# Optimization experiments

Measured on AMD Instinct MI355X. Metric: run time of the kernel, lower is better.

The kernel has to match this reference:

```python
import jax, jax.numpy as jnp
from jax import lax
import numpy as np

B, I, T, H = 128, 512, 256, 1024


def setup_inputs() -> dict:
    key = jax.random.key(0)
    k1, k2, k3, k4, k5 = jax.random.split(key, 5)
    s = 1.0 / np.sqrt(H)  # PyTorch LSTM init scale
    return {
        "x": jax.random.normal(k1, (B, I, T), jnp.float32),
        "W_ih": jax.random.uniform(k2, (4 * H, I), jnp.float32, -s, s),
        "W_hh": jax.random.uniform(k3, (4 * H, H), jnp.float32, -s, s),
        "b_ih": jax.random.uniform(k4, (4 * H,), jnp.float32, -s, s),
        "b_hh": jax.random.uniform(k5, (4 * H,), jnp.float32, -s, s),
    }


def reference(x, W_ih, W_hh, b_ih, b_hh):
    # x: [B, I, T] -> module transposes to [B, T, I]; scan over time.
    xs = jnp.transpose(x, (2, 0, 1))  # [T, B, I]
    # Precompute input projections for all timesteps (one big GEMM).
    x_proj = jnp.einsum('tbi,gi->tbg', xs, W_ih) + b_ih + b_hh  # [T, B, 4H]
    H_ = W_hh.shape[1]

    def step(carry, xp):
        h, c = carry
        gates = xp + h @ W_hh.T  # [B, 4H]
        i, f, g, o = jnp.split(gates, 4, axis=-1)  # PyTorch gate order i,f,g,o
        i = jax.nn.sigmoid(i)
        f = jax.nn.sigmoid(f)
        g = jnp.tanh(g)
        o = jax.nn.sigmoid(o)
        c = f * c + i * g
        h = o * jnp.tanh(c)
        return (h, c), None

    h0 = jnp.zeros((x.shape[0], H_), x.dtype)
    (h, _), _ = lax.scan(step, (h0, h0), x_proj)
    return h  # [B, H] == h_t.squeeze(0)
```

## Files before the change

kernel.cpp:

```cpp
#include <hip/hip_runtime.h>
#include <hip/hip_bf16.h>
#include <cstdint>
#include <cstddef>

#define B_ 128
#define I_ 512
#define T_ 256
#define H_ 1024

typedef __attribute__((ext_vector_type(8))) short short8;
typedef __attribute__((ext_vector_type(4))) float floatx4;

static __device__ __forceinline__ unsigned short f2bf(float f) {
  unsigned u = __float_as_uint(f);
  u += 0x7FFFu + ((u >> 16) & 1u);
  return (unsigned short)(u >> 16);
}
static __device__ __forceinline__ short8 pack_bf8(floatx4 a, floatx4 b) {
  short8 v;
  v[0] = (short)f2bf(a[0]); v[1] = (short)f2bf(a[1]);
  v[2] = (short)f2bf(a[2]); v[3] = (short)f2bf(a[3]);
  v[4] = (short)f2bf(b[0]); v[5] = (short)f2bf(b[1]);
  v[6] = (short)f2bf(b[2]); v[7] = (short)f2bf(b[3]);
  return v;
}

__global__ void __launch_bounds__(256) k_transpose(
    const float* __restrict__ x, unsigned short* __restrict__ xs) {
  __shared__ float tile[64][65];
  const int b  = blockIdx.x;
  const int i0 = blockIdx.y * 64;
  const int t0 = blockIdx.z * 64;
  const int tid = threadIdx.x;
  const int c = tid & 63, r4 = tid >> 6;
  const float* src = x + (size_t)b * I_ * T_ + (size_t)i0 * T_ + t0;
#pragma unroll
  for (int it = 0; it < 16; ++it) {
    const int r = it * 4 + r4;
    tile[r][c] = src[(size_t)r * T_ + c];
  }
  __syncthreads();
#pragma unroll
  for (int it = 0; it < 16; ++it) {
    const int tr = it * 4 + r4;
    xs[((size_t)(t0 + tr) * B_ + b) * I_ + i0 + c] = f2bf(tile[c][tr]);
  }
}

__global__ void __launch_bounds__(256, 1) k_lstm(
    const unsigned short* __restrict__ xs,
    const float* __restrict__ Whh,
    const float* __restrict__ Wih,
    const float* __restrict__ bih,
    const float* __restrict__ bhh,
    unsigned short* __restrict__ hring,
    float* __restrict__ out,
    unsigned int* __restrict__ flags)
{
  extern __shared__ char smem[];
  unsigned short (*hst)[32][264] = (unsigned short (*)[32][264])smem;
  float (*gx)[32][17] = (float (*)[32][17])(smem + 101376);

  const int wg = blockIdx.x, tid = threadIdx.x;
  const int lane = tid & 63, wave = tid >> 6;
  const int bt = wg & 3, jt = wg >> 2;
  const int b0 = bt * 32, j0 = jt * 16;
  const int quad = lane >> 4, cr = lane & 15;
  const size_t HBUF = (size_t)B_ * H_;

  short8 whf[32];
  {
    const float* wrow = Whh + (size_t)(wave * H_ + j0 + cr) * H_;
#pragma unroll
    for (int ks = 0; ks < 32; ++ks) {
      floatx4 wa = *(const floatx4*)(wrow + ks * 32 + quad * 8);
      floatx4 wb = *(const floatx4*)(wrow + ks * 32 + quad * 8 + 4);
      whf[ks] = pack_bf8(wa, wb);
    }
  }
  short8 wif[16];
  {
    const float* irow = Wih + (size_t)(wave * H_ + j0 + cr) * I_;
#pragma unroll
    for (int ks = 0; ks < 16; ++ks) {
      floatx4 wa = *(const floatx4*)(irow + ks * 32 + quad * 8);
      floatx4 wb = *(const floatx4*)(irow + ks * 32 + quad * 8 + 4);
      wif[ks] = pack_bf8(wa, wb);
    }
  }

  const int eb = tid >> 3;
  const int ejp = tid & 7;
  float bias[4][2];
#pragma unroll
  for (int q = 0; q < 4; ++q)
#pragma unroll
    for (int jj = 0; jj < 2; ++jj)
      bias[q][jj] = bih[q * H_ + j0 + ejp * 2 + jj] + bhh[q * H_ + j0 + ejp * 2 + jj];

  const int srow = tid >> 3;
  const int sq = tid & 7;

  float c0 = 0.f, c1 = 0.f;

  for (int t = 0; t < T_; ++t) {
    const unsigned short* hin = hring + (size_t)t * HBUF;
    unsigned short* hout = hring + (size_t)((t + 1) & 255) * HBUF;
    const unsigned short* xrow = xs + ((size_t)t * B_ + b0 + srow) * I_ + sq * 8;
    const unsigned short* hrow = hin + (size_t)(b0 + srow) * H_ + sq * 8;

    short8 xv[8];
#pragma unroll
    for (int c2 = 0; c2 < 2; ++c2)
#pragma unroll
      for (int p = 0; p < 4; ++p)
        xv[c2 * 4 + p] = *(const short8*)(xrow + c2 * 256 + p * 64);
#pragma unroll
    for (int c2 = 0; c2 < 2; ++c2)
#pragma unroll
      for (int p = 0; p < 4; ++p)
        *(short8*)&hst[c2][srow][sq * 8 + p * 64] = xv[c2 * 4 + p];
    __syncthreads();

    floatx4 accx0 = {0.f,0.f,0.f,0.f}, accx1 = {0.f,0.f,0.f,0.f};
    floatx4 aha0 = {0.f,0.f,0.f,0.f}, aha1 = {0.f,0.f,0.f,0.f};
    floatx4 ahb0 = {0.f,0.f,0.f,0.f}, ahb1 = {0.f,0.f,0.f,0.f};

    if (t > 0 && wave == 0) {
      const unsigned tgt = (unsigned)t;
      for (;;) {
        unsigned v = __hip_atomic_load(&flags[(bt + 4 * lane) * 16],
                                       __ATOMIC_RELAXED, __HIP_MEMORY_SCOPE_AGENT);
        if (__ballot(v >= tgt) == ~0ull) break;
        __builtin_amdgcn_s_sleep(1);
      }
    }

#pragma unroll
    for (int c2 = 0; c2 < 2; ++c2)
#pragma unroll
      for (int ks8 = 0; ks8 < 8; ++ks8) {
        short8 a0 = *(const short8*)&hst[c2][cr][ks8 * 32 + quad * 8];
        short8 a1 = *(const short8*)&hst[c2][16 + cr][ks8 * 32 + quad * 8];
        accx0 = __builtin_amdgcn_mfma_f32_16x16x32_bf16(a0, wif[c2 * 8 + ks8], accx0, 0, 0, 0);
        accx1 = __builtin_amdgcn_mfma_f32_16x16x32_bf16(a1, wif[c2 * 8 + ks8], accx1, 0, 0, 0);
      }
    __syncthreads();

    if (t > 0) {
      short8 hv8[16];
#pragma unroll
      for (int k = 0; k < 16; ++k)
        hv8[k] = *(const short8*)(hrow + (k >> 2) * 256 + (k & 3) * 64);

#pragma unroll
      for (int ch = 0; ch < 4; ++ch)
#pragma unroll
        for (int p = 0; p < 4; ++p)
          *(short8*)&hst[2 + ch][srow][sq * 8 + p * 64] = hv8[ch * 4 + p];
      __syncthreads();
#pragma unroll
      for (int ch = 0; ch < 4; ++ch)
#pragma unroll
        for (int ks8 = 0; ks8 < 8; ++ks8) {
          short8 a0 = *(const short8*)&hst[2 + ch][cr][ks8 * 32 + quad * 8];
          short8 a1 = *(const short8*)&hst[2 + ch][16 + cr][ks8 * 32 + quad * 8];
          if (ch < 2) {
            aha0 = __builtin_amdgcn_mfma_f32_16x16x32_bf16(a0, whf[ch * 8 + ks8], aha0, 0, 0, 0);
            aha1 = __builtin_amdgcn_mfma_f32_16x16x32_bf16(a1, whf[ch * 8 + ks8], aha1, 0, 0, 0);
          } else {
            ahb0 = __builtin_amdgcn_mfma_f32_16x16x32_bf16(a0, whf[ch * 8 + ks8], ahb0, 0, 0, 0);
            ahb1 = __builtin_amdgcn_mfma_f32_16x16x32_bf16(a1, whf[ch * 8 + ks8], ahb1, 0, 0, 0);
          }
        }
    }

#pragma unroll
    for (int r = 0; r < 4; ++r) {
      gx[wave][quad * 4 + r][cr]      = accx0[r] + aha0[r] + ahb0[r];
      gx[wave][16 + quad * 4 + r][cr] = accx1[r] + aha1[r] + ahb1[r];
    }
    __syncthreads();

    float hv0 = 0.f, hv1 = 0.f;
#pragma unroll
    for (int jj = 0; jj < 2; ++jj) {
      const int j = ejp * 2 + jj;
      float gi = gx[0][eb][j] + bias[0][jj];
      float gf = gx[1][eb][j] + bias[1][jj];
      float gg = gx[2][eb][j] + bias[2][jj];
      float go = gx[3][eb][j] + bias[3][jj];
      float si = 1.f / (1.f + __expf(-gi));
      float sf = 1.f / (1.f + __expf(-gf));
      float tg = 2.f / (1.f + __expf(-2.f * gg)) - 1.f;
      float so = 1.f / (1.f + __expf(-go));
      float& cc = jj ? c1 : c0;
      cc = sf * cc + si * tg;
      float th = 2.f / (1.f + __expf(-2.f * cc)) - 1.f;
      float hv = so * th;
      if (jj == 0) hv0 = hv; else hv1 = hv;
    }
    const unsigned hpack = (unsigned)f2bf(hv0) | ((unsigned)f2bf(hv1) << 16);
    __hip_atomic_store((unsigned*)(hout + (size_t)(b0 + eb) * H_ + j0 + ejp * 2),
                       hpack, __ATOMIC_RELAXED, __HIP_MEMORY_SCOPE_AGENT);
    if (t == T_ - 1) {
      out[(size_t)(b0 + eb) * H_ + j0 + ejp * 2 + 0] = hv0;
      out[(size_t)(b0 + eb) * H_ + j0 + ejp * 2 + 1] = hv1;
    }

    __syncthreads();
    if (tid == 0)
      __hip_atomic_store(&flags[wg * 16], (unsigned)(t + 1), __ATOMIC_RELAXED,
                         __HIP_MEMORY_SCOPE_AGENT);
  }
}

extern "C" void kernel_launch(void* const* d_in, const int* in_sizes, int n_in,
                              void* d_out, int out_size, void* d_ws, size_t ws_size,
                              hipStream_t stream) {
  (void)in_sizes; (void)n_in; (void)out_size; (void)ws_size;
  const float* x   = (const float*)d_in[0];
  const float* Wih = (const float*)d_in[1];
  const float* Whh = (const float*)d_in[2];
  const float* bih = (const float*)d_in[3];
  const float* bhh = (const float*)d_in[4];
  float* out = (float*)d_out;

  char* ws = (char*)d_ws;
  unsigned short* xs = (unsigned short*)ws;
  unsigned int*   fl = (unsigned int*)  (ws + 33554432);
  unsigned short* hring = (unsigned short*)d_in[0];

  hipMemsetAsync(fl, 0, 16384, stream);

  k_transpose<<<dim3(B_, I_ / 64, T_ / 64), 256, 0, stream>>>(x, xs);

  const int LDS_TOTAL = 110080;
  hipFuncSetAttribute((const void*)k_lstm,
                      hipFuncAttributeMaxDynamicSharedMemorySize, LDS_TOTAL);
  k_lstm<<<dim3(256), dim3(256), LDS_TOTAL, stream>>>(
      xs, Whh, Wih, bih, bhh, hring, out, fl);
}
```

Baseline: 1.158 ms.

## Split K across waves, load MFMA fragments directly from global, prefetch x

Each wave now owns a quarter of the K dimension for all four gates, instead of one gate over the full K. A-fragments for x and h are read straight from global memory into registers rather than staged through LDS, and partial sums are reduced through a small shared array in the gate stage. The next timestep's x fragment is prefetched before the flag wait, every wave polls the flags, and the flags are packed contiguously per batch tile. This removes several LDS round-trips and barriers per step on the serial recurrence path, at the cost of a larger cross-wave reduction and uncoalesced global fragment loads.

After: 1.402 ms. +21.0%, slower.

```diff
diff --git a/kernel.cpp b/kernel.cpp
--- a/kernel.cpp
+++ b/kernel.cpp
@@ -57,9 +57,7 @@
     float* __restrict__ out,
     unsigned int* __restrict__ flags)
 {
-  extern __shared__ char smem[];
-  unsigned short (*hst)[32][264] = (unsigned short (*)[32][264])smem;
-  float (*gx)[32][17] = (float (*)[32][17])(smem + 101376);
+  __shared__ float gx[4][32][67];
 
   const int wg = blockIdx.x, tid = threadIdx.x;
   const int lane = tid & 63, wave = tid >> 6;
@@ -67,25 +65,25 @@
   const int b0 = bt * 32, j0 = jt * 16;
   const int quad = lane >> 4, cr = lane & 15;
   const size_t HBUF = (size_t)B_ * H_;
-
-  short8 whf[32];
-  {
-    const float* wrow = Whh + (size_t)(wave * H_ + j0 + cr) * H_;
-#pragma unroll
-    for (int ks = 0; ks < 32; ++ks) {
+  const size_t XSTEP = (size_t)B_ * I_;
+
+  short8 whf[4][8];
+  short8 wif[4][4];
+#pragma unroll
+  for (int q = 0; q < 4; ++q) {
+    const float* wrow = Whh + (size_t)(q * H_ + j0 + cr) * H_ + wave * 256;
+#pragma unroll
+    for (int ks = 0; ks < 8; ++ks) {
       floatx4 wa = *(const floatx4*)(wrow + ks * 32 + quad * 8);
       floatx4 wb = *(const floatx4*)(wrow + ks * 32 + quad * 8 + 4);
-      whf[ks] = pack_bf8(wa, wb);
-    }
-  }
-  short8 wif[16];
-  {
-    const float* irow = Wih + (size_t)(wave * H_ + j0 + cr) * I_;
-#pragma unroll
-    for (int ks = 0; ks < 16; ++ks) {
+      whf[q][ks] = pack_bf8(wa, wb);
+    }
+    const float* irow = Wih + (size_t)(q * H_ + j0 + cr) * I_ + wave * 128;
+#pragma unroll
+    for (int ks = 0; ks < 4; ++ks) {
       floatx4 wa = *(const floatx4*)(irow + ks * 32 + quad * 8);
       floatx4 wb = *(const floatx4*)(irow + ks * 32 + quad * 8 + 4);
-      wif[ks] = pack_bf8(wa, wb);
+      wif[q][ks] = pack_bf8(wa, wb);
     }
   }
 
@@ -98,108 +96,100 @@
     for (int jj = 0; jj < 2; ++jj)
       bias[q][jj] = bih[q * H_ + j0 + ejp * 2 + jj] + bhh[q * H_ + j0 + ejp * 2 + jj];
 
-  const int srow = tid >> 3;
-  const int sq = tid & 7;
+  const unsigned short* xfrag =
+      xs + (size_t)(b0 + cr) * I_ + wave * 128 + quad * 8;
+
+  short8 xv[2][4];
+#pragma unroll
+  for (int hh = 0; hh < 2; ++hh)
+#pragma unroll
+    for (int ks = 0; ks < 4; ++ks)
+      xv[hh][ks] = *(const short8*)(xfrag + (size_t)hh * 16 * I_ + ks * 32);
 
   float c0 = 0.f, c1 = 0.f;
 
   for (int t = 0; t < T_; ++t) {
-    const unsigned short* hin = hring + (size_t)t * HBUF;
-    unsigned short* hout = hring + (size_t)((t + 1) & 255) * HBUF;
-    const unsigned short* xrow = xs + ((size_t)t * B_ + b0 + srow) * I_ + sq * 8;
-    const unsigned short* hrow = hin + (size_t)(b0 + srow) * H_ + sq * 8;
-
-    short8 xv[8];
-#pragma unroll
-    for (int c2 = 0; c2 < 2; ++c2)
-#pragma unroll
-      for (int p = 0; p < 4; ++p)
-        xv[c2 * 4 + p] = *(const short8*)(xrow + c2 * 256 + p * 64);
-#pragma unroll
-    for (int c2 = 0; c2 < 2; ++c2)
-#pragma unroll
-      for (int p = 0; p < 4; ++p)
-        *(short8*)&hst[c2][srow][sq * 8 + p * 64] = xv[c2 * 4 + p];
-    __syncthreads();
-
-    floatx4 accx0 = {0.f,0.f,0.f,0.f}, accx1 = {0.f,0.f,0.f,0.f};
-    floatx4 aha0 = {0.f,0.f,0.f,0.f}, aha1 = {0.f,0.f,0.f,0.f};
-    floatx4 ahb0 = {0.f,0.f,0.f,0.f}, ahb1 = {0.f,0.f,0.f,0.f};
-
-    if (t > 0 && wave == 0) {
+    floatx4 acc[4][2];
+#pragma unroll
+    for (int q = 0; q < 4; ++q) {
+      acc[q][0] = (floatx4){0.f, 0.f, 0.f, 0.f};
+      acc[q][1] = (floatx4){0.f, 0.f, 0.f, 0.f};
+    }
+
+#pragma unroll
+    for (int ks = 0; ks < 4; ++ks)
+#pragma unroll
+      for (int q = 0; q < 4; ++q) {
+        acc[q][0] = __builtin_amdgcn_mfma_f32_16x16x32_bf16(xv[0][ks], wif[q][ks], acc[q][0], 0, 0, 0);
+        acc[q][1] = __builtin_amdgcn_mfma_f32_16x16x32_bf16(xv[1][ks], wif[q][ks], acc[q][1], 0, 0, 0);
+      }
+
+    if (t + 1 < T_) {
+      const unsigned short* xp = xfrag + (size_t)(t + 1) * XSTEP;
+#pragma unroll
+      for (int hh = 0; hh < 2; ++hh)
+#pragma unroll
+        for (int ks = 0; ks < 4; ++ks)
+          xv[hh][ks] = *(const short8*)(xp + (size_t)hh * 16 * I_ + ks * 32);
+    }
+
+    if (t > 0) {
       const unsigned tgt = (unsigned)t;
       for (;;) {
-        unsigned v = __hip_atomic_load(&flags[(bt + 4 * lane) * 16],
+        unsigned v = __hip_atomic_load(&flags[bt * 64 + lane],
                                        __ATOMIC_RELAXED, __HIP_MEMORY_SCOPE_AGENT);
         if (__ballot(v >= tgt) == ~0ull) break;
         __builtin_amdgcn_s_sleep(1);
       }
-    }
-
-#pragma unroll
-    for (int c2 = 0; c2 < 2; ++c2)
-#pragma unroll
-      for (int ks8 = 0; ks8 < 8; ++ks8) {
-        short8 a0 = *(const short8*)&hst[c2][cr][ks8 * 32 + quad * 8];
-        short8 a1 = *(const short8*)&hst[c2][16 + cr][ks8 * 32 + quad * 8];
-        accx0 = __builtin_amdgcn_mfma_f32_16x16x32_bf16(a0, wif[c2 * 8 + ks8], accx0, 0, 0, 0);
-        accx1 = __builtin_amdgcn_mfma_f32_16x16x32_bf16(a1, wif[c2 * 8 + ks8], accx1, 0, 0, 0);
+      asm volatile("" ::: "memory");
+
+      const unsigned short* hf = hring + (size_t)t * HBUF +
+          (size_t)(b0 + cr) * H_ + wave * 256 + quad * 8;
+      short8 hv[2][8];
+#pragma unroll
+      for (int hh = 0; hh < 2; ++hh)
+#pragma unroll
+        for (int ks = 0; ks < 8; ++ks)
+          hv[hh][ks] = *(const short8*)(hf + (size_t)hh * 16 * H_ + ks * 32);
+
+#pragma unroll
+      for (int ks = 0; ks < 8; ++ks)
+#pragma unroll
+        for (int q = 0; q < 4; ++q) {
+          acc[q][0] = __builtin_amdgcn_mfma_f32_16x16x32_bf16(hv[0][ks], whf[q][ks], acc[q][0], 0, 0, 0);
+          acc[q][1] = __builtin_amdgcn_mfma_f32_16x16x32_bf16(hv[1][ks], whf[q][ks], acc[q][1], 0, 0, 0);
+        }
+    }
+
+#pragma unroll
+    for (int q = 0; q < 4; ++q)
+#pragma unroll
+      for (int r = 0; r < 4; ++r) {
+        gx[wave][quad * 4 + r][q * 16 + cr]      = acc[q][0][r];
+        gx[wave][16 + quad * 4 + r][q * 16 + cr] = acc[q][1][r];
       }
     __syncthreads();
 
-    if (t > 0) {
-      short8 hv8[16];
-#pragma unroll
-      for (int k = 0; k < 16; ++k)
-        hv8[k] = *(const short8*)(hrow + (k >> 2) * 256 + (k & 3) * 64);
-
-#pragma unroll
-      for (int ch = 0; ch < 4; ++ch)
-#pragma unroll
-        for (int p = 0; p < 4; ++p)
-          *(short8*)&hst[2 + ch][srow][sq * 8 + p * 64] = hv8[ch * 4 + p];
-      __syncthreads();
-#pragma unroll
-      for (int ch = 0; ch < 4; ++ch)
-#pragma unroll
-        for (int ks8 = 0; ks8 < 8; ++ks8) {
-          short8 a0 = *(const short8*)&hst[2 + ch][cr][ks8 * 32 + quad * 8];
-          short8 a1 = *(const short8*)&hst[2 + ch][16 + cr][ks8 * 32 + quad * 8];
-          if (ch < 2) {
-            aha0 = __builtin_amdgcn_mfma_f32_16x16x32_bf16(a0, whf[ch * 8 + ks8], aha0, 0, 0, 0);
-            aha1 = __builtin_amdgcn_mfma_f32_16x16x32_bf16(a1, whf[ch * 8 + ks8], aha1, 0, 0, 0);
-          } else {
-            ahb0 = __builtin_amdgcn_mfma_f32_16x16x32_bf16(a0, whf[ch * 8 + ks8], ahb0, 0, 0, 0);
-            ahb1 = __builtin_amdgcn_mfma_f32_16x16x32_bf16(a1, whf[ch * 8 + ks8], ahb1, 0, 0, 0);
-          }
-        }
-    }
-
-#pragma unroll
-    for (int r = 0; r < 4; ++r) {
-      gx[wave][quad * 4 + r][cr]      = accx0[r] + aha0[r] + ahb0[r];
-      gx[wave][16 + quad * 4 + r][cr] = accx1[r] + aha1[r] + ahb1[r];
-    }
-    __syncthreads();
-
     float hv0 = 0.f, hv1 = 0.f;
 #pragma unroll
     for (int jj = 0; jj < 2; ++jj) {
       const int j = ejp * 2 + jj;
-      float gi = gx[0][eb][j] + bias[0][jj];
-      float gf = gx[1][eb][j] + bias[1][jj];
-      float gg = gx[2][eb][j] + bias[2][jj];
-      float go = gx[3][eb][j] + bias[3][jj];
-      float si = 1.f / (1.f + __expf(-gi));
-      float sf = 1.f / (1.f + __expf(-gf));
-      float tg = 2.f / (1.f + __expf(-2.f * gg)) - 1.f;
-      float so = 1.f / (1.f + __expf(-go));
+      float g[4];
+#pragma unroll
+      for (int q = 0; q < 4; ++q)
+        g[q] = gx[0][eb][q * 16 + j] + gx[1][eb][q * 16 + j] +
+               gx[2][eb][q * 16 + j] + gx[3][eb][q * 16 + j] + bias[q][jj];
+      float si = 1.f / (1.f + __expf(-g[0]));
+      float sf = 1.f / (1.f + __expf(-g[1]));
+      float tg = 2.f / (1.f + __expf(-2.f * g[2])) - 1.f;
+      float so = 1.f / (1.f + __expf(-g[3]));
       float& cc = jj ? c1 : c0;
       cc = sf * cc + si * tg;
       float th = 2.f / (1.f + __expf(-2.f * cc)) - 1.f;
-      float hv = so * th;
-      if (jj == 0) hv0 = hv; else hv1 = hv;
-    }
+      float hvv = so * th;
+      if (jj == 0) hv0 = hvv; else hv1 = hvv;
+    }
+    unsigned short* hout = hring + (size_t)((t + 1) & 255) * HBUF;
     const unsigned hpack = (unsigned)f2bf(hv0) | ((unsigned)f2bf(hv1) << 16);
     __hip_atomic_store((unsigned*)(hout + (size_t)(b0 + eb) * H_ + j0 + ejp * 2),
                        hpack, __ATOMIC_RELAXED, __HIP_MEMORY_SCOPE_AGENT);
@@ -210,8 +200,8 @@
 
     __syncthreads();
     if (tid == 0)
-      __hip_atomic_store(&flags[wg * 16], (unsigned)(t + 1), __ATOMIC_RELAXED,
-                         __HIP_MEMORY_SCOPE_AGENT);
+      __hip_atomic_store(&flags[bt * 64 + jt], (unsigned)(t + 1),
+                         __ATOMIC_RELAXED, __HIP_MEMORY_SCOPE_AGENT);
   }
 }
 
@@ -235,9 +225,6 @@
 
   k_transpose<<<dim3(B_, I_ / 64, T_ / 64), 256, 0, stream>>>(x, xs);
 
-  const int LDS_TOTAL = 110080;
-  hipFuncSetAttribute((const void*)k_lstm,
-                      hipFuncAttributeMaxDynamicSharedMemorySize, LDS_TOTAL);
-  k_lstm<<<dim3(256), dim3(256), LDS_TOTAL, stream>>>(
+  k_lstm<<<dim3(256), dim3(256), 0, stream>>>(
       xs, Whh, Wih, bih, bhh, hring, out, fl);
 }
```

## Use per-wave completion flags, prefetch next-step x, and drop barriers in LSTM loop

Applied to the files above, without the earlier changes.

Each wave now publishes its own completion flag after waiting for its stores to drain, rather than the whole workgroup barriering before thread 0 publishes. Every wave spins on its own producers' flags, and the recurrent h loads are issued right after that wait so they overlap with the input-projection MFMAs. Next-timestep x rows are prefetched into registers one step ahead, and two __syncthreads per step are removed. This shortens the per-timestep serial critical path. In exchange it causes four times more flag polling traffic and relies on relaxed atomics plus manual waitcnt for cross-workgroup ordering.

Result: slower. 1.516 ms (+30.9%).

```diff
diff --git a/kernel.cpp b/kernel.cpp
--- a/kernel.cpp
+++ b/kernel.cpp
@@ -67,6 +67,7 @@
   const int b0 = bt * 32, j0 = jt * 16;
   const int quad = lane >> 4, cr = lane & 15;
   const size_t HBUF = (size_t)B_ * H_;
+  const size_t XSTEP = (size_t)B_ * I_;
 
   short8 whf[32];
   {
@@ -101,39 +102,57 @@
   const int srow = tid >> 3;
   const int sq = tid & 7;
 
+  const unsigned short* xbase = xs + (size_t)(b0 + srow) * I_ + sq * 8;
+
+  short8 xv[8];
+#pragma unroll
+  for (int c2 = 0; c2 < 2; ++c2)
+#pragma unroll
+    for (int p = 0; p < 4; ++p)
+      xv[c2 * 4 + p] = *(const short8*)(xbase + c2 * 256 + p * 64);
+
   float c0 = 0.f, c1 = 0.f;
 
   for (int t = 0; t < T_; ++t) {
-    const unsigned short* hin = hring + (size_t)t * HBUF;
-    unsigned short* hout = hring + (size_t)((t + 1) & 255) * HBUF;
-    const unsigned short* xrow = xs + ((size_t)t * B_ + b0 + srow) * I_ + sq * 8;
-    const unsigned short* hrow = hin + (size_t)(b0 + srow) * H_ + sq * 8;
-
-    short8 xv[8];
-#pragma unroll
-    for (int c2 = 0; c2 < 2; ++c2)
-#pragma unroll
-      for (int p = 0; p < 4; ++p)
-        xv[c2 * 4 + p] = *(const short8*)(xrow + c2 * 256 + p * 64);
 #pragma unroll
     for (int c2 = 0; c2 < 2; ++c2)
 #pragma unroll
       for (int p = 0; p < 4; ++p)
         *(short8*)&hst[c2][srow][sq * 8 + p * 64] = xv[c2 * 4 + p];
+    if (t + 1 < T_) {
+      const unsigned short* xp = xbase + (size_t)(t + 1) * XSTEP;
+#pragma unroll
+      for (int c2 = 0; c2 < 2; ++c2)
+#pragma unroll
+        for (int p = 0; p < 4; ++p)
+          xv[c2 * 4 + p] = *(const short8*)(xp + c2 * 256 + p * 64);
+    }
     __syncthreads();
 
     floatx4 accx0 = {0.f,0.f,0.f,0.f}, accx1 = {0.f,0.f,0.f,0.f};
     floatx4 aha0 = {0.f,0.f,0.f,0.f}, aha1 = {0.f,0.f,0.f,0.f};
     floatx4 ahb0 = {0.f,0.f,0.f,0.f}, ahb1 = {0.f,0.f,0.f,0.f};
 
-    if (t > 0 && wave == 0) {
+    short8 hv8[16];
+    if (t > 0) {
       const unsigned tgt = (unsigned)t;
+      const unsigned int* fb = flags + (size_t)(bt + 4 * lane) * 16;
       for (;;) {
-        unsigned v = __hip_atomic_load(&flags[(bt + 4 * lane) * 16],
-                                       __ATOMIC_RELAXED, __HIP_MEMORY_SCOPE_AGENT);
-        if (__ballot(v >= tgt) == ~0ull) break;
+        unsigned v0 = __hip_atomic_load(fb + 0, __ATOMIC_RELAXED, __HIP_MEMORY_SCOPE_AGENT);
+        unsigned v1 = __hip_atomic_load(fb + 1, __ATOMIC_RELAXED, __HIP_MEMORY_SCOPE_AGENT);
+        unsigned v2 = __hip_atomic_load(fb + 2, __ATOMIC_RELAXED, __HIP_MEMORY_SCOPE_AGENT);
+        unsigned v3 = __hip_atomic_load(fb + 3, __ATOMIC_RELAXED, __HIP_MEMORY_SCOPE_AGENT);
+        bool ok = (v0 >= tgt) & (v1 >= tgt) & (v2 >= tgt) & (v3 >= tgt);
+        if (__ballot(ok) == ~0ull) break;
         __builtin_amdgcn_s_sleep(1);
       }
+      asm volatile("" ::: "memory");
+
+      const unsigned short* hrow = hring + (size_t)t * HBUF +
+                                   (size_t)(b0 + srow) * H_ + sq * 8;
+#pragma unroll
+      for (int k = 0; k < 16; ++k)
+        hv8[k] = *(const short8*)(hrow + (k >> 2) * 256 + (k & 3) * 64);
     }
 
 #pragma unroll
@@ -145,14 +164,8 @@
         accx0 = __builtin_amdgcn_mfma_f32_16x16x32_bf16(a0, wif[c2 * 8 + ks8], accx0, 0, 0, 0);
         accx1 = __builtin_amdgcn_mfma_f32_16x16x32_bf16(a1, wif[c2 * 8 + ks8], accx1, 0, 0, 0);
       }
-    __syncthreads();
 
     if (t > 0) {
-      short8 hv8[16];
-#pragma unroll
-      for (int k = 0; k < 16; ++k)
-        hv8[k] = *(const short8*)(hrow + (k >> 2) * 256 + (k & 3) * 64);
-
 #pragma unroll
       for (int ch = 0; ch < 4; ++ch)
 #pragma unroll
@@ -200,6 +213,7 @@
       float hv = so * th;
       if (jj == 0) hv0 = hv; else hv1 = hv;
     }
+    unsigned short* hout = hring + (size_t)((t + 1) & 255) * HBUF;
     const unsigned hpack = (unsigned)f2bf(hv0) | ((unsigned)f2bf(hv1) << 16);
     __hip_atomic_store((unsigned*)(hout + (size_t)(b0 + eb) * H_ + j0 + ejp * 2),
                        hpack, __ATOMIC_RELAXED, __HIP_MEMORY_SCOPE_AGENT);
@@ -208,10 +222,10 @@
       out[(size_t)(b0 + eb) * H_ + j0 + ejp * 2 + 1] = hv1;
     }
 
-    __syncthreads();
-    if (tid == 0)
-      __hip_atomic_store(&flags[wg * 16], (unsigned)(t + 1), __ATOMIC_RELAXED,
-                         __HIP_MEMORY_SCOPE_AGENT);
+    asm volatile("s_waitcnt vmcnt(0)" ::: "memory");
+    if (lane == 0)
+      __hip_atomic_store(&flags[wg * 16 + wave], (unsigned)(t + 1),
+                         __ATOMIC_RELAXED, __HIP_MEMORY_SCOPE_AGENT);
   }
 }
 
```

## Switch LSTM recurrence to 32x32x16 MFMA with split-K across wave pairs

Applied to the files above, without the earlier changes.

Replaces the 16x16x32 bf16 MFMA tiles with 32x32x16 MFMAs. Each wave now computes two gates over 32 batch rows for half of the K dimension, and the partial sums from the wave pairs are reduced through LDS in the gate nonlinearity stage. The aim is to halve the LDS A-operand reads per wave and use the larger MFMA shape for better throughput on the serial per-step critical path. The gx buffer grows to hold 32 columns, which raises LDS use, and each gate now needs an extra cross-wave add.

Result: faster. 1.079 ms (-6.9%).

```diff
diff --git a/kernel.cpp b/kernel.cpp
--- a/kernel.cpp
+++ b/kernel.cpp
@@ -10,6 +10,7 @@
 
 typedef __attribute__((ext_vector_type(8))) short short8;
 typedef __attribute__((ext_vector_type(4))) float floatx4;
+typedef __attribute__((ext_vector_type(16))) float floatx16;
 
 static __device__ __forceinline__ unsigned short f2bf(float f) {
   unsigned u = __float_as_uint(f);
@@ -23,6 +24,10 @@
   v[4] = (short)f2bf(b[0]); v[5] = (short)f2bf(b[1]);
   v[6] = (short)f2bf(b[2]); v[7] = (short)f2bf(b[3]);
   return v;
+}
+static __device__ __forceinline__ floatx16 zero16() {
+  return (floatx16){0.f,0.f,0.f,0.f,0.f,0.f,0.f,0.f,
+                    0.f,0.f,0.f,0.f,0.f,0.f,0.f,0.f};
 }
 
 __global__ void __launch_bounds__(256) k_transpose(
@@ -59,33 +64,37 @@
 {
   extern __shared__ char smem[];
   unsigned short (*hst)[32][264] = (unsigned short (*)[32][264])smem;
-  float (*gx)[32][17] = (float (*)[32][17])(smem + 101376);
+  float (*gx)[32][33] = (float (*)[32][33])(smem + 101376);
 
   const int wg = blockIdx.x, tid = threadIdx.x;
   const int lane = tid & 63, wave = tid >> 6;
+  const int gp = wave >> 1, kh = wave & 1;
   const int bt = wg & 3, jt = wg >> 2;
   const int b0 = bt * 32, j0 = jt * 16;
-  const int quad = lane >> 4, cr = lane & 15;
+  const int arow = lane & 31;
+  const int hi = lane >> 5;
+  const int gate = gp * 2 + (arow >> 4);
+  const int wcol = j0 + (arow & 15);
   const size_t HBUF = (size_t)B_ * H_;
 
   short8 whf[32];
   {
-    const float* wrow = Whh + (size_t)(wave * H_ + j0 + cr) * H_;
-#pragma unroll
-    for (int ks = 0; ks < 32; ++ks) {
-      floatx4 wa = *(const floatx4*)(wrow + ks * 32 + quad * 8);
-      floatx4 wb = *(const floatx4*)(wrow + ks * 32 + quad * 8 + 4);
-      whf[ks] = pack_bf8(wa, wb);
+    const float* wrow = Whh + (size_t)(gate * H_ + wcol) * H_ + kh * 512;
+#pragma unroll
+    for (int kc = 0; kc < 32; ++kc) {
+      floatx4 wa = *(const floatx4*)(wrow + kc * 16 + hi * 8);
+      floatx4 wb = *(const floatx4*)(wrow + kc * 16 + hi * 8 + 4);
+      whf[kc] = pack_bf8(wa, wb);
     }
   }
   short8 wif[16];
   {
-    const float* irow = Wih + (size_t)(wave * H_ + j0 + cr) * I_;
-#pragma unroll
-    for (int ks = 0; ks < 16; ++ks) {
-      floatx4 wa = *(const floatx4*)(irow + ks * 32 + quad * 8);
-      floatx4 wb = *(const floatx4*)(irow + ks * 32 + quad * 8 + 4);
-      wif[ks] = pack_bf8(wa, wb);
+    const float* irow = Wih + (size_t)(gate * H_ + wcol) * I_ + kh * 256;
+#pragma unroll
+    for (int kc = 0; kc < 16; ++kc) {
+      floatx4 wa = *(const floatx4*)(irow + kc * 16 + hi * 8);
+      floatx4 wb = *(const floatx4*)(irow + kc * 16 + hi * 8 + 4);
+      wif[kc] = pack_bf8(wa, wb);
     }
   }
 
@@ -122,9 +131,8 @@
         *(short8*)&hst[c2][srow][sq * 8 + p * 64] = xv[c2 * 4 + p];
     __syncthreads();
 
-    floatx4 accx0 = {0.f,0.f,0.f,0.f}, accx1 = {0.f,0.f,0.f,0.f};
-    floatx4 aha0 = {0.f,0.f,0.f,0.f}, aha1 = {0.f,0.f,0.f,0.f};
-    floatx4 ahb0 = {0.f,0.f,0.f,0.f}, ahb1 = {0.f,0.f,0.f,0.f};
+    floatx16 accxa = zero16(), accxb = zero16();
+    floatx16 ah0 = zero16(), ah1 = zero16();
 
     if (t > 0 && wave == 0) {
       const unsigned tgt = (unsigned)t;
@@ -137,14 +145,13 @@
     }
 
 #pragma unroll
-    for (int c2 = 0; c2 < 2; ++c2)
-#pragma unroll
-      for (int ks8 = 0; ks8 < 8; ++ks8) {
-        short8 a0 = *(const short8*)&hst[c2][cr][ks8 * 32 + quad * 8];
-        short8 a1 = *(const short8*)&hst[c2][16 + cr][ks8 * 32 + quad * 8];
-        accx0 = __builtin_amdgcn_mfma_f32_16x16x32_bf16(a0, wif[c2 * 8 + ks8], accx0, 0, 0, 0);
-        accx1 = __builtin_amdgcn_mfma_f32_16x16x32_bf16(a1, wif[c2 * 8 + ks8], accx1, 0, 0, 0);
-      }
+    for (int kc = 0; kc < 16; ++kc) {
+      short8 a = *(const short8*)&hst[kh][arow][kc * 16 + hi * 8];
+      if (kc & 1)
+        accxb = __builtin_amdgcn_mfma_f32_32x32x16_bf16(a, wif[kc], accxb, 0, 0, 0);
+      else
+        accxa = __builtin_amdgcn_mfma_f32_32x32x16_bf16(a, wif[kc], accxa, 0, 0, 0);
+    }
     __syncthreads();
 
     if (t > 0) {
@@ -160,25 +167,21 @@
           *(short8*)&hst[2 + ch][srow][sq * 8 + p * 64] = hv8[ch * 4 + p];
       __syncthreads();
 #pragma unroll
-      for (int ch = 0; ch < 4; ++ch)
-#pragma unroll
-        for (int ks8 = 0; ks8 < 8; ++ks8) {
-          short8 a0 = *(const short8*)&hst[2 + ch][cr][ks8 * 32 + quad * 8];
-          short8 a1 = *(const short8*)&hst[2 + ch][16 + cr][ks8 * 32 + quad * 8];
-          if (ch < 2) {
-            aha0 = __builtin_amdgcn_mfma_f32_16x16x32_bf16(a0, whf[ch * 8 + ks8], aha0, 0, 0, 0);
-            aha1 = __builtin_amdgcn_mfma_f32_16x16x32_bf16(a1, whf[ch * 8 + ks8], aha1, 0, 0, 0);
-          } else {
-            ahb0 = __builtin_amdgcn_mfma_f32_16x16x32_bf16(a0, whf[ch * 8 + ks8], ahb0, 0, 0, 0);
-            ahb1 = __builtin_amdgcn_mfma_f32_16x16x32_bf16(a1, whf[ch * 8 + ks8], ahb1, 0, 0, 0);
-          }
+      for (int ch2 = 0; ch2 < 2; ++ch2)
+#pragma unroll
+        for (int kc = 0; kc < 16; ++kc) {
+          short8 a = *(const short8*)&hst[2 + 2 * kh + ch2][arow][kc * 16 + hi * 8];
+          if (ch2 == 0)
+            ah0 = __builtin_amdgcn_mfma_f32_32x32x16_bf16(a, whf[kc], ah0, 0, 0, 0);
+          else
+            ah1 = __builtin_amdgcn_mfma_f32_32x32x16_bf16(a, whf[16 + kc], ah1, 0, 0, 0);
         }
     }
 
 #pragma unroll
-    for (int r = 0; r < 4; ++r) {
-      gx[wave][quad * 4 + r][cr]      = accx0[r] + aha0[r] + ahb0[r];
-      gx[wave][16 + quad * 4 + r][cr] = accx1[r] + aha1[r] + ahb1[r];
+    for (int r = 0; r < 16; ++r) {
+      const int row = (r & 3) + 8 * (r >> 2) + 4 * hi;
+      gx[wave][row][arow] = accxa[r] + accxb[r] + ah0[r] + ah1[r];
     }
     __syncthreads();
 
@@ -186,10 +189,10 @@
 #pragma unroll
     for (int jj = 0; jj < 2; ++jj) {
       const int j = ejp * 2 + jj;
-      float gi = gx[0][eb][j] + bias[0][jj];
-      float gf = gx[1][eb][j] + bias[1][jj];
-      float gg = gx[2][eb][j] + bias[2][jj];
-      float go = gx[3][eb][j] + bias[3][jj];
+      float gi = gx[0][eb][j]      + gx[1][eb][j]      + bias[0][jj];
+      float gf = gx[0][eb][16 + j] + gx[1][eb][16 + j] + bias[1][jj];
+      float gg = gx[2][eb][j]      + gx[3][eb][j]      + bias[2][jj];
+      float go = gx[2][eb][16 + j] + gx[3][eb][16 + j] + bias[3][jj];
       float si = 1.f / (1.f + __expf(-gi));
       float sf = 1.f / (1.f + __expf(-gf));
       float tg = 2.f / (1.f + __expf(-2.f * gg)) - 1.f;
@@ -235,7 +238,7 @@
 
   k_transpose<<<dim3(B_, I_ / 64, T_ / 64), 256, 0, stream>>>(x, xs);
 
-  const int LDS_TOTAL = 110080;
+  const int LDS_TOTAL = 118272;
   hipFuncSetAttribute((const void*)k_lstm,
                       hipFuncAttributeMaxDynamicSharedMemorySize, LDS_TOTAL);
   k_lstm<<<dim3(256), dim3(256), LDS_TOTAL, stream>>>(
```
